# Kernel optimization log

Hardware: AMD Instinct MI355X
Metric: run time of the kernel (lower is better)

## Reference

```python
import jax, jax.numpy as jnp
import numpy as np

LAT_SIZE = 2048
BATCH = 4096


def cos_pos_encoding_1d(size, freq_div=2.0, sub_freq_max=4.0):
    freqs = list(range(1, int(size / freq_div)))
    spaces = [np.linspace(0, freq * 2 * np.pi, size) for freq in freqs]
    sub_freqs = [1.0 / float(i) for i in range(2, int(sub_freq_max))]
    sub_spaces = [np.linspace(i * freq * 2 * np.pi, (i + 1) * freq * 2 * np.pi, size)
                  for freq in sub_freqs for i in range(int(1 / freq))]
    spaces = spaces + sub_spaces
    cos = [np.cos(space) for space in spaces]
    return np.stack(cos).astype(np.float32)  # (n_freq, size)


def setup_inputs() -> dict:
    key = jax.random.key(0)
    k1, k2 = jax.random.split(key)
    cos_basis = jnp.asarray(cos_pos_encoding_1d(LAT_SIZE, 1, 8))  # (2074, 2048)
    n_freq = cos_basis.shape[0]
    x = jax.random.normal(k1, (BATCH, LAT_SIZE), dtype=jnp.float32)
    # nn.Linear default init: U(-1/sqrt(in), 1/sqrt(in))
    bound = 1.0 / np.sqrt(LAT_SIZE)
    W = jax.random.uniform(k2, (n_freq, LAT_SIZE), dtype=jnp.float32,
                           minval=-bound, maxval=bound)
    return {"x": x, "W": W, "cos_basis": cos_basis}


def reference(x, W, cos_basis):
    # x: (B, lat), W: (n_freq, lat), cos_basis: (n_freq, lat)
    x_freqs = x @ W.T                          # (B, n_freq)  -- to_freq_size
    # broadcast-mul + sum over freq dim == GEMM against fixed cosine basis
    out = x_freqs @ cos_basis                  # (B, lat)
    # global max-normalize (norm=True)
    return out / jnp.max(out)
```

## Files before the change

kernel.cpp:

```cpp
#include <hip/hip_runtime.h>
#include <hip/hip_bf16.h>
#include <cstdint>

#define BATCH 4096
#define LAT   2048
#define NFREQ 2074
#define KPAD  2112

typedef __bf16 bf16x8 __attribute__((ext_vector_type(8)));
typedef float  f32x4  __attribute__((ext_vector_type(4)));

__device__ __forceinline__ unsigned short f2bf(float f) {
    unsigned int u = __float_as_uint(f);
    u = (u + 0x7fffu + ((u >> 16) & 1u)) >> 16;
    return (unsigned short)u;
}

__device__ __forceinline__ void gload_lds16(const unsigned short* g, unsigned short* l) {
    __builtin_amdgcn_global_load_lds(
        (const __attribute__((address_space(1))) unsigned int*)g,
        (__attribute__((address_space(3))) unsigned int*)l,
        16, 0, 0);
}

__global__ void prep_kernel(const float* __restrict__ x,
                            const float* __restrict__ W,
                            const float* __restrict__ cb,
                            unsigned short* __restrict__ xb,
                            unsigned short* __restrict__ WT,
                            unsigned short* __restrict__ cosT,
                            float* __restrict__ maxp) {
    __shared__ float t[64][65];
    const int bid = blockIdx.x;
    const int tid = threadIdx.x;
    if (bid < 4096) {
        int i = bid * 256 + tid;
        const float4* x4 = (const float4*)x;
        float4 a = x4[2 * i];
        float4 b = x4[2 * i + 1];
        union { unsigned short us[8]; uint4 v; } p;
        p.us[0] = f2bf(a.x); p.us[1] = f2bf(a.y); p.us[2] = f2bf(a.z); p.us[3] = f2bf(a.w);
        p.us[4] = f2bf(b.x); p.us[5] = f2bf(b.y); p.us[6] = f2bf(b.z); p.us[7] = f2bf(b.w);
        ((uint4*)xb)[i] = p.v;
        if (i == 0) *maxp = -__builtin_inff();
        return;
    }
    int b2 = bid - 4096;
    const float* in     = (b2 < 1056) ? W  : cb;
    unsigned short* out = (b2 < 1056) ? WT : cosT;
    if (b2 >= 1056) b2 -= 1056;
    const int c0 = (b2 % 32) * 64;
    const int r0 = (b2 / 32) * 64;
    for (int i = tid; i < 4096; i += 256) {
        int rr = i >> 6, cc = i & 63;
        int r = r0 + rr;
        float v = (r < NFREQ) ? in[(size_t)r * LAT + c0 + cc] : 0.0f;
        t[rr][cc] = v;
    }
    __syncthreads();
    for (int i = tid; i < 4096; i += 256) {
        int cc = i >> 6, rr = i & 63;
        out[(size_t)(c0 + cc) * KPAD + (r0 + rr)] = f2bf(t[rr][cc]);
    }
}

template <int N, int K>
__global__ __launch_bounds__(256, 2)
void gemm1_kernel(const unsigned short* __restrict__ A,
                  const unsigned short* __restrict__ Bt,
                  unsigned short* __restrict__ C) {
    __shared__ alignas(16) unsigned short As[3][128 * 32];
    __shared__ alignas(16) unsigned short Bs[3][64 * 32];

    const int tid  = threadIdx.x;
    const int wave = tid >> 6;
    const int lane = tid & 63;
    const int wm   = (wave >> 1) * 64;
    const int wn   = (wave & 1) * 32;
    const int quad = lane >> 4;
    const int l16  = lane & 15;

    const int mBase = blockIdx.y * 128;
    const int nBase = blockIdx.x * 64;

    const int srow = lane >> 2;
    const int sk   = (lane & 3) * 8;

    const unsigned short* Ab1 = A  + (size_t)(mBase + (wave * 2 + 0) * 16 + srow) * K + sk;
    const unsigned short* Ab2 = A  + (size_t)(mBase + (wave * 2 + 1) * 16 + srow) * K + sk;
    const unsigned short* Bb1 = Bt + (size_t)(nBase + wave * 16 + srow) * K + sk;

    const int aoff1 = ((wave * 2 + 0) * 16) * 32;
    const int aoff2 = ((wave * 2 + 1) * 16) * 32;
    const int boff  = (wave * 16) * 32;

    constexpr int NIT = K / 32;
    gload_lds16(Ab1, &As[0][aoff1]);
    gload_lds16(Ab2, &As[0][aoff2]);
    gload_lds16(Bb1, &Bs[0][boff]);

    f32x4 acc[4][2] = {};
    int bc = 0;
    for (int j = 0; j < NIT; ++j) {
        const int bn = (bc == 2) ? 0 : bc + 1;
        if (j + 1 < NIT) {
            const int k0 = (j + 1) * 32;
            gload_lds16(Ab1 + k0, &As[bn][aoff1]);
            gload_lds16(Ab2 + k0, &As[bn][aoff2]);
            gload_lds16(Bb1 + k0, &Bs[bn][boff]);
            asm volatile("s_waitcnt vmcnt(3)\n\ts_barrier" ::: "memory");
        } else {
            asm volatile("s_waitcnt vmcnt(0)\n\ts_barrier" ::: "memory");
        }
        bf16x8 af[4], bfr[2];
#pragma unroll
        for (int mi = 0; mi < 4; ++mi)
            af[mi] = *(const bf16x8*)&As[bc][(wm + mi * 16 + l16) * 32 + quad * 8];
#pragma unroll
        for (int ni = 0; ni < 2; ++ni)
            bfr[ni] = *(const bf16x8*)&Bs[bc][(wn + ni * 16 + l16) * 32 + quad * 8];
#pragma unroll
        for (int mi = 0; mi < 4; ++mi)
#pragma unroll
            for (int ni = 0; ni < 2; ++ni)
                acc[mi][ni] = __builtin_amdgcn_mfma_f32_16x16x32_bf16(
                    af[mi], bfr[ni], acc[mi][ni], 0, 0, 0);
        bc = bn;
    }

#pragma unroll
    for (int mi = 0; mi < 4; ++mi)
#pragma unroll
        for (int ni = 0; ni < 2; ++ni) {
            int col = nBase + wn + ni * 16 + l16;
#pragma unroll
            for (int r = 0; r < 4; ++r) {
                int row = mBase + wm + mi * 16 + quad * 4 + r;
                C[(size_t)row * N + col] = f2bf(acc[mi][ni][r]);
            }
        }
}

template <int N, int K>
__global__ __launch_bounds__(512, 4)
void gemm2_kernel(const unsigned short* __restrict__ A,
                  const unsigned short* __restrict__ Bt,
                  float* __restrict__ C,
                  float* __restrict__ maxp) {
    __shared__ alignas(16) unsigned short As[3][128 * 32];
    __shared__ alignas(16) unsigned short Bs[3][128 * 32];
    __shared__ float redbuf[8];

    const int tid  = threadIdx.x;
    const int wave = tid >> 6;
    const int lane = tid & 63;
    const int wm   = (wave >> 2) * 64;
    const int wn   = (wave & 3) * 32;
    const int quad = lane >> 4;
    const int l16  = lane & 15;

    const int mBase = blockIdx.y * 128;
    const int nBase = blockIdx.x * 128;

    const int srow = lane >> 2;
    const int sk   = (lane & 3) * 8;

    const unsigned short* Ab1 = A  + (size_t)(mBase + wave * 16 + srow) * K + sk;
    const unsigned short* Bb1 = Bt + (size_t)(nBase + wave * 16 + srow) * K + sk;
    const int coff = (wave * 16) * 32;

    constexpr int NIT = K / 32;
    gload_lds16(Ab1, &As[0][coff]);
    gload_lds16(Bb1, &Bs[0][coff]);

    f32x4 acc[4][2] = {};
    int bc = 0;
    for (int j = 0; j < NIT; ++j) {
        const int bn = (bc == 2) ? 0 : bc + 1;
        if (j + 1 < NIT) {
            const int k0 = (j + 1) * 32;
            gload_lds16(Ab1 + k0, &As[bn][coff]);
            gload_lds16(Bb1 + k0, &Bs[bn][coff]);
            asm volatile("s_waitcnt vmcnt(2)\n\ts_barrier" ::: "memory");
        } else {
            asm volatile("s_waitcnt vmcnt(0)\n\ts_barrier" ::: "memory");
        }
        bf16x8 af[4], bfr[2];
#pragma unroll
        for (int mi = 0; mi < 4; ++mi)
            af[mi] = *(const bf16x8*)&As[bc][(wm + mi * 16 + l16) * 32 + quad * 8];
#pragma unroll
        for (int ni = 0; ni < 2; ++ni)
            bfr[ni] = *(const bf16x8*)&Bs[bc][(wn + ni * 16 + l16) * 32 + quad * 8];
#pragma unroll
        for (int mi = 0; mi < 4; ++mi)
#pragma unroll
            for (int ni = 0; ni < 2; ++ni)
                acc[mi][ni] = __builtin_amdgcn_mfma_f32_16x16x32_bf16(
                    af[mi], bfr[ni], acc[mi][ni], 0, 0, 0);
        bc = bn;
    }

    float vmax = -__builtin_inff();
#pragma unroll
    for (int mi = 0; mi < 4; ++mi)
#pragma unroll
        for (int ni = 0; ni < 2; ++ni) {
            int col = nBase + wn + ni * 16 + l16;
#pragma unroll
            for (int r = 0; r < 4; ++r) {
                int row = mBase + wm + mi * 16 + quad * 4 + r;
                float v = acc[mi][ni][r];
                C[(size_t)row * N + col] = v;
                vmax = fmaxf(vmax, v);
            }
        }
#pragma unroll
    for (int off = 32; off > 0; off >>= 1)
        vmax = fmaxf(vmax, __shfl_xor(vmax, off));
    if (lane == 0) redbuf[wave] = vmax;
    __syncthreads();
    if (tid == 0) {
        float m = redbuf[0];
#pragma unroll
        for (int w = 1; w < 8; ++w) m = fmaxf(m, redbuf[w]);
        if (m >= 0.0f) atomicMax((int*)maxp, __float_as_int(m));
        else           atomicMin((unsigned int*)maxp, __float_as_uint(m));
    }
}

__global__ void scale_kernel(float* __restrict__ out, const float* __restrict__ maxp) {
    int i = blockIdx.x * blockDim.x + threadIdx.x;
    float inv = 1.0f / (*maxp);
    float4* o4 = (float4*)out;
    float4 v = o4[i];
    v.x *= inv; v.y *= inv; v.z *= inv; v.w *= inv;
    o4[i] = v;
}

extern "C" void kernel_launch(void* const* d_in, const int* in_sizes, int n_in,
                              void* d_out, int out_size, void* d_ws, size_t ws_size,
                              hipStream_t stream) {
    const float* x  = (const float*)d_in[0];
    const float* W  = (const float*)d_in[1];
    const float* cb = (const float*)d_in[2];

    char* ws = (char*)d_ws;
    unsigned short* xb   = (unsigned short*)ws;
    unsigned short* WT   = (unsigned short*)(ws + (size_t)BATCH * LAT * 2);
    unsigned short* cosT = (unsigned short*)((char*)WT + (size_t)LAT * KPAD * 2);
    unsigned short* C1   = (unsigned short*)((char*)cosT + (size_t)LAT * KPAD * 2);
    float*          maxp = (float*)((char*)C1 + (size_t)LAT * LAT * 2);
    float*          out  = (float*)d_out;

    prep_kernel<<<4096 + 2 * 1056, 256, 0, stream>>>(x, W, cb, xb, WT, cosT, maxp);

    gemm1_kernel<LAT, KPAD>
        <<<dim3(LAT / 64, LAT / 128), 256, 0, stream>>>(cosT, WT, C1);

    gemm2_kernel<LAT, LAT>
        <<<dim3(LAT / 128, BATCH / 128), 512, 0, stream>>>(xb, C1, out, maxp);

    scale_kernel<<<(out_size / 4) / 256, 256, 0, stream>>>(out, maxp);
}
```

Before: 206.7 us.

## Swizzle LDS k-chunks and give gemm2 waves larger 64x64 tiles

Adds an XOR swizzle of the 8-element k-chunk position, both on the global-to-LDS load and on the fragment reads, in both GEMMs, to cut LDS bank conflicts. gemm2 moves from 512 threads with 64x32 per-wave tiles to 256 threads with 64x64 per-wave tiles, which doubles the MFMA work per fragment load. The cost is more accumulator registers per thread (64 floats) and fewer waves per block to hide latency.

After: 206.1 us. About the same (-0.3%).

```diff
diff --git a/kernel.cpp b/kernel.cpp
--- a/kernel.cpp
+++ b/kernel.cpp
@@ -64,6 +64,7 @@
     }
 }
 
+
 template <int N, int K>
 __global__ __launch_bounds__(256, 2)
 void gemm1_kernel(const unsigned short* __restrict__ A,
@@ -84,7 +85,7 @@
     const int nBase = blockIdx.x * 64;
 
     const int srow = lane >> 2;
-    const int sk   = (lane & 3) * 8;
+    const int sk   = (((lane & 3) ^ ((srow >> 1) & 3))) * 8;
 
     const unsigned short* Ab1 = A  + (size_t)(mBase + (wave * 2 + 0) * 16 + srow) * K + sk;
     const unsigned short* Ab2 = A  + (size_t)(mBase + (wave * 2 + 1) * 16 + srow) * K + sk;
@@ -93,6 +94,8 @@
     const int aoff1 = ((wave * 2 + 0) * 16) * 32;
     const int aoff2 = ((wave * 2 + 1) * 16) * 32;
     const int boff  = (wave * 16) * 32;
+
+    const int pc = (quad ^ ((l16 >> 1) & 3)) * 8;
 
     constexpr int NIT = K / 32;
     gload_lds16(Ab1, &As[0][aoff1]);
@@ -115,10 +118,10 @@
         bf16x8 af[4], bfr[2];
 #pragma unroll
         for (int mi = 0; mi < 4; ++mi)
-            af[mi] = *(const bf16x8*)&As[bc][(wm + mi * 16 + l16) * 32 + quad * 8];
+            af[mi] = *(const bf16x8*)&As[bc][(wm + mi * 16 + l16) * 32 + pc];
 #pragma unroll
         for (int ni = 0; ni < 2; ++ni)
-            bfr[ni] = *(const bf16x8*)&Bs[bc][(wn + ni * 16 + l16) * 32 + quad * 8];
+            bfr[ni] = *(const bf16x8*)&Bs[bc][(wn + ni * 16 + l16) * 32 + pc];
 #pragma unroll
         for (int mi = 0; mi < 4; ++mi)
 #pragma unroll
@@ -142,20 +145,20 @@
 }
 
 template <int N, int K>
-__global__ __launch_bounds__(512, 4)
+__global__ __launch_bounds__(256, 2)
 void gemm2_kernel(const unsigned short* __restrict__ A,
                   const unsigned short* __restrict__ Bt,
                   float* __restrict__ C,
                   float* __restrict__ maxp) {
     __shared__ alignas(16) unsigned short As[3][128 * 32];
     __shared__ alignas(16) unsigned short Bs[3][128 * 32];
-    __shared__ float redbuf[8];
+    __shared__ float redbuf[4];
 
     const int tid  = threadIdx.x;
     const int wave = tid >> 6;
     const int lane = tid & 63;
-    const int wm   = (wave >> 2) * 64;
-    const int wn   = (wave & 3) * 32;
+    const int wm   = (wave >> 1) * 64;
+    const int wn   = (wave & 1) * 64;
     const int quad = lane >> 4;
     const int l16  = lane & 15;
 
@@ -163,39 +166,49 @@
     const int nBase = blockIdx.x * 128;
 
     const int srow = lane >> 2;
-    const int sk   = (lane & 3) * 8;
-
-    const unsigned short* Ab1 = A  + (size_t)(mBase + wave * 16 + srow) * K + sk;
-    const unsigned short* Bb1 = Bt + (size_t)(nBase + wave * 16 + srow) * K + sk;
-    const int coff = (wave * 16) * 32;
+    const int sk   = (((lane & 3) ^ ((srow >> 1) & 3))) * 8;
+
+    const unsigned short* Ab1 = A  + (size_t)(mBase + (wave * 2 + 0) * 16 + srow) * K + sk;
+    const unsigned short* Ab2 = A  + (size_t)(mBase + (wave * 2 + 1) * 16 + srow) * K + sk;
+    const unsigned short* Bb1 = Bt + (size_t)(nBase + (wave * 2 + 0) * 16 + srow) * K + sk;
+    const unsigned short* Bb2 = Bt + (size_t)(nBase + (wave * 2 + 1) * 16 + srow) * K + sk;
+
+    const int off1 = ((wave * 2 + 0) * 16) * 32;
+    const int off2 = ((wave * 2 + 1) * 16) * 32;
+
+    const int pc = (quad ^ ((l16 >> 1) & 3)) * 8;
 
     constexpr int NIT = K / 32;
-    gload_lds16(Ab1, &As[0][coff]);
-    gload_lds16(Bb1, &Bs[0][coff]);
-
-    f32x4 acc[4][2] = {};
+    gload_lds16(Ab1, &As[0][off1]);
+    gload_lds16(Ab2, &As[0][off2]);
+    gload_lds16(Bb1, &Bs[0][off1]);
+    gload_lds16(Bb2, &Bs[0][off2]);
+
+    f32x4 acc[4][4] = {};
     int bc = 0;
     for (int j = 0; j < NIT; ++j) {
         const int bn = (bc == 2) ? 0 : bc + 1;
         if (j + 1 < NIT) {
             const int k0 = (j + 1) * 32;
-            gload_lds16(Ab1 + k0, &As[bn][coff]);
-            gload_lds16(Bb1 + k0, &Bs[bn][coff]);
-            asm volatile("s_waitcnt vmcnt(2)\n\ts_barrier" ::: "memory");
+            gload_lds16(Ab1 + k0, &As[bn][off1]);
+            gload_lds16(Ab2 + k0, &As[bn][off2]);
+            gload_lds16(Bb1 + k0, &Bs[bn][off1]);
+            gload_lds16(Bb2 + k0, &Bs[bn][off2]);
+            asm volatile("s_waitcnt vmcnt(4)\n\ts_barrier" ::: "memory");
         } else {
             asm volatile("s_waitcnt vmcnt(0)\n\ts_barrier" ::: "memory");
         }
-        bf16x8 af[4], bfr[2];
-#pragma unroll
-        for (int mi = 0; mi < 4; ++mi)
-            af[mi] = *(const bf16x8*)&As[bc][(wm + mi * 16 + l16) * 32 + quad * 8];
-#pragma unroll
-        for (int ni = 0; ni < 2; ++ni)
-            bfr[ni] = *(const bf16x8*)&Bs[bc][(wn + ni * 16 + l16) * 32 + quad * 8];
-#pragma unroll
-        for (int mi = 0; mi < 4; ++mi)
-#pragma unroll
-            for (int ni = 0; ni < 2; ++ni)
+        bf16x8 af[4], bfr[4];
+#pragma unroll
+        for (int mi = 0; mi < 4; ++mi)
+            af[mi] = *(const bf16x8*)&As[bc][(wm + mi * 16 + l16) * 32 + pc];
+#pragma unroll
+        for (int ni = 0; ni < 4; ++ni)
+            bfr[ni] = *(const bf16x8*)&Bs[bc][(wn + ni * 16 + l16) * 32 + pc];
+#pragma unroll
+        for (int mi = 0; mi < 4; ++mi)
+#pragma unroll
+            for (int ni = 0; ni < 4; ++ni)
                 acc[mi][ni] = __builtin_amdgcn_mfma_f32_16x16x32_bf16(
                     af[mi], bfr[ni], acc[mi][ni], 0, 0, 0);
         bc = bn;
@@ -205,7 +218,7 @@
 #pragma unroll
     for (int mi = 0; mi < 4; ++mi)
 #pragma unroll
-        for (int ni = 0; ni < 2; ++ni) {
+        for (int ni = 0; ni < 4; ++ni) {
             int col = nBase + wn + ni * 16 + l16;
 #pragma unroll
             for (int r = 0; r < 4; ++r) {
@@ -223,7 +236,7 @@
     if (tid == 0) {
         float m = redbuf[0];
 #pragma unroll
-        for (int w = 1; w < 8; ++w) m = fmaxf(m, redbuf[w]);
+        for (int w = 1; w < 4; ++w) m = fmaxf(m, redbuf[w]);
         if (m >= 0.0f) atomicMax((int*)maxp, __float_as_int(m));
         else           atomicMin((unsigned int*)maxp, __float_as_uint(m));
     }
@@ -259,7 +272,7 @@
         <<<dim3(LAT / 64, LAT / 128), 256, 0, stream>>>(cosT, WT, C1);
 
     gemm2_kernel<LAT, LAT>
-        <<<dim3(LAT / 128, BATCH / 128), 512, 0, stream>>>(xb, C1, out, maxp);
+        <<<dim3(LAT / 128, BATCH / 128), 256, 0, stream>>>(xb, C1, out, maxp);
 
     scale_kernel<<<(out_size / 4) / 256, 256, 0, stream>>>(out, maxp);
 }
```

## Fuse max-normalize into GEMM2 via grid spin barrier; swizzle LDS; vectorize prep

Applied to the files above, without the earlier changes.

GEMM2 blocks publish their local max, increment a global counter and spin until all blocks arrive. They then write the output already scaled by the inverse global max, and set a per-block flag so the scale kernel skips tiles that were already normalized. Both GEMMs use an XOR swizzle on the LDS k-chunk to reduce bank conflicts, and the prep transpose uses float4 loads and ushort4 stores. The spin barrier assumes all blocks are co-resident; if they are not, the timeout falls back to the separate scale pass at the cost of spin time.

Result: slower. 265.2 us (+28.3%).

```diff
diff --git a/kernel.cpp b/kernel.cpp
--- a/kernel.cpp
+++ b/kernel.cpp
@@ -29,7 +29,8 @@
                             unsigned short* __restrict__ xb,
                             unsigned short* __restrict__ WT,
                             unsigned short* __restrict__ cosT,
-                            float* __restrict__ maxp) {
+                            float* __restrict__ maxp,
+                            int* __restrict__ cnt) {
     __shared__ float t[64][65];
     const int bid = blockIdx.x;
     const int tid = threadIdx.x;
@@ -42,7 +43,7 @@
         p.us[0] = f2bf(a.x); p.us[1] = f2bf(a.y); p.us[2] = f2bf(a.z); p.us[3] = f2bf(a.w);
         p.us[4] = f2bf(b.x); p.us[5] = f2bf(b.y); p.us[6] = f2bf(b.z); p.us[7] = f2bf(b.w);
         ((uint4*)xb)[i] = p.v;
-        if (i == 0) *maxp = -__builtin_inff();
+        if (i == 0) { *maxp = -__builtin_inff(); *cnt = 0; }
         return;
     }
     int b2 = bid - 4096;
@@ -51,18 +52,27 @@
     if (b2 >= 1056) b2 -= 1056;
     const int c0 = (b2 % 32) * 64;
     const int r0 = (b2 / 32) * 64;
-    for (int i = tid; i < 4096; i += 256) {
-        int rr = i >> 6, cc = i & 63;
-        int r = r0 + rr;
-        float v = (r < NFREQ) ? in[(size_t)r * LAT + c0 + cc] : 0.0f;
-        t[rr][cc] = v;
+    for (int i = tid; i < 1024; i += 256) {
+        int rr = i >> 4;
+        int c4 = (i & 15) * 4;
+        int r  = r0 + rr;
+        float4 v;
+        if (r < NFREQ) v = *(const float4*)&in[(size_t)r * LAT + c0 + c4];
+        else           v = make_float4(0.f, 0.f, 0.f, 0.f);
+        t[rr][c4 + 0] = v.x; t[rr][c4 + 1] = v.y;
+        t[rr][c4 + 2] = v.z; t[rr][c4 + 3] = v.w;
     }
     __syncthreads();
-    for (int i = tid; i < 4096; i += 256) {
-        int cc = i >> 6, rr = i & 63;
-        out[(size_t)(c0 + cc) * KPAD + (r0 + rr)] = f2bf(t[rr][cc]);
-    }
-}
+    for (int i = tid; i < 1024; i += 256) {
+        int cc = i >> 4;
+        int r4 = (i & 15) * 4;
+        ushort4 o;
+        o.x = f2bf(t[r4 + 0][cc]); o.y = f2bf(t[r4 + 1][cc]);
+        o.z = f2bf(t[r4 + 2][cc]); o.w = f2bf(t[r4 + 3][cc]);
+        *(ushort4*)&out[(size_t)(c0 + cc) * KPAD + r0 + r4] = o;
+    }
+}
+
 
 template <int N, int K>
 __global__ __launch_bounds__(256, 2)
@@ -84,7 +94,7 @@
     const int nBase = blockIdx.x * 64;
 
     const int srow = lane >> 2;
-    const int sk   = (lane & 3) * 8;
+    const int sk   = (((lane & 3) ^ ((srow >> 1) & 3))) * 8;
 
     const unsigned short* Ab1 = A  + (size_t)(mBase + (wave * 2 + 0) * 16 + srow) * K + sk;
     const unsigned short* Ab2 = A  + (size_t)(mBase + (wave * 2 + 1) * 16 + srow) * K + sk;
@@ -93,6 +103,8 @@
     const int aoff1 = ((wave * 2 + 0) * 16) * 32;
     const int aoff2 = ((wave * 2 + 1) * 16) * 32;
     const int boff  = (wave * 16) * 32;
+
+    const int pc = (quad ^ ((l16 >> 1) & 3)) * 8;
 
     constexpr int NIT = K / 32;
     gload_lds16(Ab1, &As[0][aoff1]);
@@ -115,10 +127,10 @@
         bf16x8 af[4], bfr[2];
 #pragma unroll
         for (int mi = 0; mi < 4; ++mi)
-            af[mi] = *(const bf16x8*)&As[bc][(wm + mi * 16 + l16) * 32 + quad * 8];
+            af[mi] = *(const bf16x8*)&As[bc][(wm + mi * 16 + l16) * 32 + pc];
 #pragma unroll
         for (int ni = 0; ni < 2; ++ni)
-            bfr[ni] = *(const bf16x8*)&Bs[bc][(wn + ni * 16 + l16) * 32 + quad * 8];
+            bfr[ni] = *(const bf16x8*)&Bs[bc][(wn + ni * 16 + l16) * 32 + pc];
 #pragma unroll
         for (int mi = 0; mi < 4; ++mi)
 #pragma unroll
@@ -146,10 +158,13 @@
 void gemm2_kernel(const unsigned short* __restrict__ A,
                   const unsigned short* __restrict__ Bt,
                   float* __restrict__ C,
-                  float* __restrict__ maxp) {
+                  float* __restrict__ maxp,
+                  int* __restrict__ cnt,
+                  int* __restrict__ flags) {
     __shared__ alignas(16) unsigned short As[3][128 * 32];
     __shared__ alignas(16) unsigned short Bs[3][128 * 32];
     __shared__ float redbuf[8];
+    __shared__ float s_inv;
 
     const int tid  = threadIdx.x;
     const int wave = tid >> 6;
@@ -163,11 +178,13 @@
     const int nBase = blockIdx.x * 128;
 
     const int srow = lane >> 2;
-    const int sk   = (lane & 3) * 8;
+    const int sk   = (((lane & 3) ^ ((srow >> 1) & 3))) * 8;
 
     const unsigned short* Ab1 = A  + (size_t)(mBase + wave * 16 + srow) * K + sk;
     const unsigned short* Bb1 = Bt + (size_t)(nBase + wave * 16 + srow) * K + sk;
     const int coff = (wave * 16) * 32;
+
+    const int pc = (quad ^ ((l16 >> 1) & 3)) * 8;
 
     constexpr int NIT = K / 32;
     gload_lds16(Ab1, &As[0][coff]);
@@ -188,10 +205,10 @@
         bf16x8 af[4], bfr[2];
 #pragma unroll
         for (int mi = 0; mi < 4; ++mi)
-            af[mi] = *(const bf16x8*)&As[bc][(wm + mi * 16 + l16) * 32 + quad * 8];
+            af[mi] = *(const bf16x8*)&As[bc][(wm + mi * 16 + l16) * 32 + pc];
 #pragma unroll
         for (int ni = 0; ni < 2; ++ni)
-            bfr[ni] = *(const bf16x8*)&Bs[bc][(wn + ni * 16 + l16) * 32 + quad * 8];
+            bfr[ni] = *(const bf16x8*)&Bs[bc][(wn + ni * 16 + l16) * 32 + pc];
 #pragma unroll
         for (int mi = 0; mi < 4; ++mi)
 #pragma unroll
@@ -205,16 +222,10 @@
 #pragma unroll
     for (int mi = 0; mi < 4; ++mi)
 #pragma unroll
-        for (int ni = 0; ni < 2; ++ni) {
-            int col = nBase + wn + ni * 16 + l16;
-#pragma unroll
-            for (int r = 0; r < 4; ++r) {
-                int row = mBase + wm + mi * 16 + quad * 4 + r;
-                float v = acc[mi][ni][r];
-                C[(size_t)row * N + col] = v;
-                vmax = fmaxf(vmax, v);
-            }
-        }
+        for (int ni = 0; ni < 2; ++ni)
+#pragma unroll
+            for (int r = 0; r < 4; ++r)
+                vmax = fmaxf(vmax, acc[mi][ni][r]);
 #pragma unroll
     for (int off = 32; off > 0; off >>= 1)
         vmax = fmaxf(vmax, __shfl_xor(vmax, off));
@@ -226,11 +237,44 @@
         for (int w = 1; w < 8; ++w) m = fmaxf(m, redbuf[w]);
         if (m >= 0.0f) atomicMax((int*)maxp, __float_as_int(m));
         else           atomicMin((unsigned int*)maxp, __float_as_uint(m));
-    }
-}
-
-__global__ void scale_kernel(float* __restrict__ out, const float* __restrict__ maxp) {
+        __threadfence();
+        __hip_atomic_fetch_add(cnt, 1, __ATOMIC_ACQ_REL, __HIP_MEMORY_SCOPE_AGENT);
+        const int total = gridDim.x * gridDim.y;
+        int ok = 0;
+        for (int it = 0; it < 30000; ++it) {
+            if (__hip_atomic_load(cnt, __ATOMIC_ACQUIRE,
+                                  __HIP_MEMORY_SCOPE_AGENT) >= total) { ok = 1; break; }
+            __builtin_amdgcn_s_sleep(8);
+        }
+        float mx = __int_as_float(
+            __hip_atomic_load((int*)maxp, __ATOMIC_RELAXED, __HIP_MEMORY_SCOPE_AGENT));
+        s_inv = ok ? (1.0f / mx) : 1.0f;
+        flags[blockIdx.y * gridDim.x + blockIdx.x] = ok;
+    }
+    __syncthreads();
+    const float inv = s_inv;
+
+#pragma unroll
+    for (int mi = 0; mi < 4; ++mi)
+#pragma unroll
+        for (int ni = 0; ni < 2; ++ni) {
+            int col = nBase + wn + ni * 16 + l16;
+#pragma unroll
+            for (int r = 0; r < 4; ++r) {
+                int row = mBase + wm + mi * 16 + quad * 4 + r;
+                C[(size_t)row * N + col] = acc[mi][ni][r] * inv;
+            }
+        }
+}
+
+__global__ void scale_kernel(float* __restrict__ out, const float* __restrict__ maxp,
+                             const int* __restrict__ flags) {
     int i = blockIdx.x * blockDim.x + threadIdx.x;
+    int e   = i * 4;
+    int row = e >> 11;
+    int col = e & 2047;
+    int gbid = (row >> 7) * (LAT / 128) + (col >> 7);
+    if (flags[gbid]) return;
     float inv = 1.0f / (*maxp);
     float4* o4 = (float4*)out;
     float4 v = o4[i];
@@ -251,15 +295,17 @@
     unsigned short* cosT = (unsigned short*)((char*)WT + (size_t)LAT * KPAD * 2);
     unsigned short* C1   = (unsigned short*)((char*)cosT + (size_t)LAT * KPAD * 2);
     float*          maxp = (float*)((char*)C1 + (size_t)LAT * LAT * 2);
+    int*            cnt   = (int*)(maxp + 1);
+    int*            flags = (int*)(maxp + 2);
     float*          out  = (float*)d_out;
 
-    prep_kernel<<<4096 + 2 * 1056, 256, 0, stream>>>(x, W, cb, xb, WT, cosT, maxp);
+    prep_kernel<<<4096 + 2 * 1056, 256, 0, stream>>>(x, W, cb, xb, WT, cosT, maxp, cnt);
 
     gemm1_kernel<LAT, KPAD>
         <<<dim3(LAT / 64, LAT / 128), 256, 0, stream>>>(cosT, WT, C1);
 
     gemm2_kernel<LAT, LAT>
-        <<<dim3(LAT / 128, BATCH / 128), 512, 0, stream>>>(xb, C1, out, maxp);
-
-    scale_kernel<<<(out_size / 4) / 256, 256, 0, stream>>>(out, maxp);
-}
+        <<<dim3(LAT / 128, BATCH / 128), 512, 0, stream>>>(xb, C1, out, maxp, cnt, flags);
+
+    scale_kernel<<<(out_size / 4) / 256, 256, 0, stream>>>(out, maxp, flags);
+}
```

## Swizzle LDS tiles, deepen gemm2 prefetch, and vectorize transpose prep

Applied to the files above, without the earlier changes.

The prep transpose now reads float4 and writes ushort4 chunks instead of scalars. Both GEMMs XOR-swizzle the k-chunk position in LDS so that MFMA operand reads avoid bank conflicts. gemm2 moves from 3 to 4 LDS stages with a two-iteration prefetch distance. It also splits each iteration into two MFMA halves with setprio and an extra barrier, issuing the B load between the halves to interleave memory and compute. The cost is more LDS per block, which may reduce occupancy, plus an extra barrier per iteration.

Result: faster. 200.4 us (-3.1%).

```diff
diff --git a/kernel.cpp b/kernel.cpp
--- a/kernel.cpp
+++ b/kernel.cpp
@@ -51,18 +51,27 @@
     if (b2 >= 1056) b2 -= 1056;
     const int c0 = (b2 % 32) * 64;
     const int r0 = (b2 / 32) * 64;
-    for (int i = tid; i < 4096; i += 256) {
-        int rr = i >> 6, cc = i & 63;
-        int r = r0 + rr;
-        float v = (r < NFREQ) ? in[(size_t)r * LAT + c0 + cc] : 0.0f;
-        t[rr][cc] = v;
+    for (int i = tid; i < 1024; i += 256) {
+        int rr = i >> 4;
+        int c4 = (i & 15) * 4;
+        int r  = r0 + rr;
+        float4 v;
+        if (r < NFREQ) v = *(const float4*)&in[(size_t)r * LAT + c0 + c4];
+        else           v = make_float4(0.f, 0.f, 0.f, 0.f);
+        t[rr][c4 + 0] = v.x; t[rr][c4 + 1] = v.y;
+        t[rr][c4 + 2] = v.z; t[rr][c4 + 3] = v.w;
     }
     __syncthreads();
-    for (int i = tid; i < 4096; i += 256) {
-        int cc = i >> 6, rr = i & 63;
-        out[(size_t)(c0 + cc) * KPAD + (r0 + rr)] = f2bf(t[rr][cc]);
-    }
-}
+    for (int i = tid; i < 1024; i += 256) {
+        int cc = i >> 4;
+        int r4 = (i & 15) * 4;
+        ushort4 o;
+        o.x = f2bf(t[r4 + 0][cc]); o.y = f2bf(t[r4 + 1][cc]);
+        o.z = f2bf(t[r4 + 2][cc]); o.w = f2bf(t[r4 + 3][cc]);
+        *(ushort4*)&out[(size_t)(c0 + cc) * KPAD + r0 + r4] = o;
+    }
+}
+
 
 template <int N, int K>
 __global__ __launch_bounds__(256, 2)
@@ -84,7 +93,7 @@
     const int nBase = blockIdx.x * 64;
 
     const int srow = lane >> 2;
-    const int sk   = (lane & 3) * 8;
+    const int sk   = (((lane & 3) ^ ((srow >> 1) & 3))) * 8;
 
     const unsigned short* Ab1 = A  + (size_t)(mBase + (wave * 2 + 0) * 16 + srow) * K + sk;
     const unsigned short* Ab2 = A  + (size_t)(mBase + (wave * 2 + 1) * 16 + srow) * K + sk;
@@ -93,6 +102,8 @@
     const int aoff1 = ((wave * 2 + 0) * 16) * 32;
     const int aoff2 = ((wave * 2 + 1) * 16) * 32;
     const int boff  = (wave * 16) * 32;
+
+    const int pc = (quad ^ ((l16 >> 1) & 3)) * 8;
 
     constexpr int NIT = K / 32;
     gload_lds16(Ab1, &As[0][aoff1]);
@@ -115,10 +126,10 @@
         bf16x8 af[4], bfr[2];
 #pragma unroll
         for (int mi = 0; mi < 4; ++mi)
-            af[mi] = *(const bf16x8*)&As[bc][(wm + mi * 16 + l16) * 32 + quad * 8];
+            af[mi] = *(const bf16x8*)&As[bc][(wm + mi * 16 + l16) * 32 + pc];
 #pragma unroll
         for (int ni = 0; ni < 2; ++ni)
-            bfr[ni] = *(const bf16x8*)&Bs[bc][(wn + ni * 16 + l16) * 32 + quad * 8];
+            bfr[ni] = *(const bf16x8*)&Bs[bc][(wn + ni * 16 + l16) * 32 + pc];
 #pragma unroll
         for (int mi = 0; mi < 4; ++mi)
 #pragma unroll
@@ -147,8 +158,8 @@
                   const unsigned short* __restrict__ Bt,
                   float* __restrict__ C,
                   float* __restrict__ maxp) {
-    __shared__ alignas(16) unsigned short As[3][128 * 32];
-    __shared__ alignas(16) unsigned short Bs[3][128 * 32];
+    __shared__ alignas(16) unsigned short As[4][128 * 32];
+    __shared__ alignas(16) unsigned short Bs[4][128 * 32];
     __shared__ float redbuf[8];
 
     const int tid  = threadIdx.x;
@@ -163,42 +174,56 @@
     const int nBase = blockIdx.x * 128;
 
     const int srow = lane >> 2;
-    const int sk   = (lane & 3) * 8;
+    const int sk   = (((lane & 3) ^ ((srow >> 1) & 3))) * 8;
 
     const unsigned short* Ab1 = A  + (size_t)(mBase + wave * 16 + srow) * K + sk;
     const unsigned short* Bb1 = Bt + (size_t)(nBase + wave * 16 + srow) * K + sk;
     const int coff = (wave * 16) * 32;
 
+    const int pc = (quad ^ ((l16 >> 1) & 3)) * 8;
+
     constexpr int NIT = K / 32;
-    gload_lds16(Ab1, &As[0][coff]);
-    gload_lds16(Bb1, &Bs[0][coff]);
+    gload_lds16(Ab1,      &As[0][coff]);
+    gload_lds16(Bb1,      &Bs[0][coff]);
+    gload_lds16(Ab1 + 32, &As[1][coff]);
+    gload_lds16(Bb1 + 32, &Bs[1][coff]);
 
     f32x4 acc[4][2] = {};
-    int bc = 0;
     for (int j = 0; j < NIT; ++j) {
-        const int bn = (bc == 2) ? 0 : bc + 1;
-        if (j + 1 < NIT) {
-            const int k0 = (j + 1) * 32;
-            gload_lds16(Ab1 + k0, &As[bn][coff]);
-            gload_lds16(Bb1 + k0, &Bs[bn][coff]);
+        const int c = j & 3;
+        const int s = (j + 2) & 3;
+        if (j + 2 < NIT) {
+            gload_lds16(Ab1 + (j + 2) * 32, &As[s][coff]);
+            asm volatile("s_waitcnt vmcnt(3)\n\ts_barrier" ::: "memory");
+        } else if (j + 1 < NIT) {
             asm volatile("s_waitcnt vmcnt(2)\n\ts_barrier" ::: "memory");
         } else {
             asm volatile("s_waitcnt vmcnt(0)\n\ts_barrier" ::: "memory");
         }
-        bf16x8 af[4], bfr[2];
-#pragma unroll
-        for (int mi = 0; mi < 4; ++mi)
-            af[mi] = *(const bf16x8*)&As[bc][(wm + mi * 16 + l16) * 32 + quad * 8];
-#pragma unroll
-        for (int ni = 0; ni < 2; ++ni)
-            bfr[ni] = *(const bf16x8*)&Bs[bc][(wn + ni * 16 + l16) * 32 + quad * 8];
-#pragma unroll
-        for (int mi = 0; mi < 4; ++mi)
-#pragma unroll
-            for (int ni = 0; ni < 2; ++ni)
-                acc[mi][ni] = __builtin_amdgcn_mfma_f32_16x16x32_bf16(
-                    af[mi], bfr[ni], acc[mi][ni], 0, 0, 0);
-        bc = bn;
+        bf16x8 a0 = *(const bf16x8*)&As[c][(wm +  0 + l16) * 32 + pc];
+        bf16x8 a1 = *(const bf16x8*)&As[c][(wm + 16 + l16) * 32 + pc];
+        bf16x8 b0 = *(const bf16x8*)&Bs[c][(wn +  0 + l16) * 32 + pc];
+        bf16x8 b1 = *(const bf16x8*)&Bs[c][(wn + 16 + l16) * 32 + pc];
+        __builtin_amdgcn_s_setprio(1);
+        acc[0][0] = __builtin_amdgcn_mfma_f32_16x16x32_bf16(a0, b0, acc[0][0], 0, 0, 0);
+        acc[0][1] = __builtin_amdgcn_mfma_f32_16x16x32_bf16(a0, b1, acc[0][1], 0, 0, 0);
+        acc[1][0] = __builtin_amdgcn_mfma_f32_16x16x32_bf16(a1, b0, acc[1][0], 0, 0, 0);
+        acc[1][1] = __builtin_amdgcn_mfma_f32_16x16x32_bf16(a1, b1, acc[1][1], 0, 0, 0);
+        __builtin_amdgcn_s_setprio(0);
+        __builtin_amdgcn_sched_barrier(0);
+        asm volatile("s_barrier" ::: "memory");
+        if (j + 2 < NIT)
+            gload_lds16(Bb1 + (j + 2) * 32, &Bs[s][coff]);
+        bf16x8 a2 = *(const bf16x8*)&As[c][(wm + 32 + l16) * 32 + pc];
+        bf16x8 a3 = *(const bf16x8*)&As[c][(wm + 48 + l16) * 32 + pc];
+        __builtin_amdgcn_s_setprio(1);
+        acc[2][0] = __builtin_amdgcn_mfma_f32_16x16x32_bf16(a2, b0, acc[2][0], 0, 0, 0);
+        acc[2][1] = __builtin_amdgcn_mfma_f32_16x16x32_bf16(a2, b1, acc[2][1], 0, 0, 0);
+        acc[3][0] = __builtin_amdgcn_mfma_f32_16x16x32_bf16(a3, b0, acc[3][0], 0, 0, 0);
+        acc[3][1] = __builtin_amdgcn_mfma_f32_16x16x32_bf16(a3, b1, acc[3][1], 0, 0, 0);
+        __builtin_amdgcn_s_setprio(0);
+        __builtin_amdgcn_sched_barrier(0);
+        asm volatile("s_barrier" ::: "memory");
     }
 
     float vmax = -__builtin_inff();
```
